# Optimization experiments

Hardware: AMD Instinct MI355X
Metric: run time of the kernel (lower is better)

Reference implementation:

```python
import jax, jax.numpy as jnp
import numpy as np

N = 2_097_152
NUM_DIM = 4
NUM_FACTOR = 32
VOCABS = {"dow": 7, "time": 24, "sex": 2, "age": 100, "month": 12, "day": 31}
NUM_DEST = 100_000


def setup_inputs() -> dict:
    key = jax.random.key(0)
    ks = jax.random.split(key, 16)
    inp = {}
    # forward index args
    names = ["dayofweek", "time", "sex", "age", "month", "day"]
    maxes = [7, 24, 2, 100, 12, 31]
    for i, (n, m) in enumerate(zip(names, maxes)):
        inp[n] = jax.random.randint(ks[i], (N,), 0, m, dtype=jnp.int64 if jax.config.jax_enable_x64 else jnp.int32)
    inp["destination"] = jax.random.randint(ks[6], (N,), 0, NUM_DEST, dtype=jnp.int32)
    # learned params (all feature embeddings ~ N(0,1) like nn.init.normal_)
    inp["emb_dow"] = jax.random.normal(ks[7], (7, NUM_DIM), jnp.float32)
    inp["emb_time"] = jax.random.normal(ks[8], (24, NUM_DIM), jnp.float32)
    inp["emb_sex"] = jax.random.normal(ks[9], (2, NUM_DIM), jnp.float32)
    inp["emb_age"] = jax.random.normal(ks[10], (100, NUM_DIM), jnp.float32)
    inp["emb_month"] = jax.random.normal(ks[11], (12, NUM_DIM), jnp.float32)
    inp["emb_day"] = jax.random.normal(ks[12], (31, NUM_DIM), jnp.float32)
    # user projection Linear(6*num_dim -> num_factor)
    fan_in = 6 * NUM_DIM
    bound = 1.0 / np.sqrt(fan_in)
    inp["W"] = jax.random.uniform(ks[13], (fan_in, NUM_FACTOR), jnp.float32, -bound, bound)
    inp["b"] = jax.random.uniform(ks[14], (NUM_FACTOR,), jnp.float32, -bound, bound)
    inp["item_table"] = jax.random.normal(ks[15], (NUM_DEST, NUM_FACTOR), jnp.float32)
    return inp


def reference(dayofweek, time, sex, age, month, day, destination,
              emb_dow, emb_time, emb_sex, emb_age, emb_month, emb_day,
              W, b, item_table):
    # user embedding: gather 6 feature embeddings, concat -> [N, 24], project -> [N, 32]
    u = jnp.concatenate([
        emb_dow[dayofweek], emb_time[time], emb_sex[sex],
        emb_age[age], emb_month[month], emb_day[day],
    ], axis=-1)
    user = u @ W + b                      # [N, F]
    item = item_table[destination]        # [N, F]
    # diag(user @ item^T) == row-wise dot product (same math, O(N) not O(N^2))
    return jnp.sum(user * item, axis=-1)  # [N]
```

## Files before the change

kernel.cpp:

```cpp
#include <hip/hip_runtime.h>


#define NF 32
#define LDS_STRIDE 36
#define NV 176

__device__ __forceinline__ float4 ldsf4(const float* p) {
    return *reinterpret_cast<const float4*>(p);
}

__device__ __forceinline__ float dot4(float4 u, float4 v, float a) {
    a = fmaf(u.x, v.x, a);
    a = fmaf(u.y, v.y, a);
    a = fmaf(u.z, v.z, a);
    a = fmaf(u.w, v.w, a);
    return a;
}

#define QUAD(IV, Q)                                                  \
    acc0 = dot4(ldsf4(&proj[b0 + (Q) * 4]), IV, acc0);               \
    acc1 = dot4(ldsf4(&proj[b1 + (Q) * 4]), IV, acc1);               \
    acc2 = dot4(ldsf4(&proj[b2 + (Q) * 4]), IV, acc2);               \
    acc0 = dot4(ldsf4(&proj[b3 + (Q) * 4]), IV, acc0);               \
    acc1 = dot4(ldsf4(&proj[b4 + (Q) * 4]), IV, acc1);               \
    acc2 = dot4(ldsf4(&proj[b5 + (Q) * 4]), IV, acc2);

#define NTL(P) __builtin_nontemporal_load(P)

__global__ __launch_bounds__(256, 4)
void mf_kernel(const int* __restrict__ dow, const int* __restrict__ tmi,
               const int* __restrict__ sx,  const int* __restrict__ ag,
               const int* __restrict__ mo,  const int* __restrict__ dy,
               const int* __restrict__ dst,
               const float* __restrict__ e_dow,   const float* __restrict__ e_time,
               const float* __restrict__ e_sex,   const float* __restrict__ e_age,
               const float* __restrict__ e_month, const float* __restrict__ e_day,
               const float* __restrict__ W, const float* __restrict__ bvec,
               const float* __restrict__ item_table,
               float* __restrict__ out, int n)
{
    __shared__ float proj[NV * LDS_STRIDE];

    const int tid = threadIdx.x;
    for (int t = tid; t < NV * NF; t += blockDim.x) {
        int entry = t >> 5;
        int f     = t & 31;
        int k, v;
        const float* e;
        if      (entry < 7)   { k = 0; v = entry;       e = e_dow;   }
        else if (entry < 31)  { k = 1; v = entry - 7;   e = e_time;  }
        else if (entry < 33)  { k = 2; v = entry - 31;  e = e_sex;   }
        else if (entry < 133) { k = 3; v = entry - 33;  e = e_age;   }
        else if (entry < 145) { k = 4; v = entry - 133; e = e_month; }
        else                  { k = 5; v = entry - 145; e = e_day;   }
        float acc = (k == 0) ? bvec[f] : 0.0f;
        #pragma unroll
        for (int d = 0; d < 4; ++d)
            acc += e[v * 4 + d] * W[(k * 4 + d) * NF + f];
        proj[entry * LDS_STRIDE + f] = acc;
    }
    __syncthreads();

    const int tstride = gridDim.x * blockDim.x;
    int i = blockIdx.x * blockDim.x + tid;
    if (i >= n) return;

    int j0 = NTL(&dow[i]), j1 = NTL(&tmi[i]), j2 = NTL(&sx[i]),
        j3 = NTL(&ag[i]),  j4 = NTL(&mo[i]),  j5 = NTL(&dy[i]),
        jd = NTL(&dst[i]);

    for (;;) {
        const int b0 = (0   + j0) * LDS_STRIDE;
        const int b1 = (7   + j1) * LDS_STRIDE;
        const int b2 = (31  + j2) * LDS_STRIDE;
        const int b3 = (33  + j3) * LDS_STRIDE;
        const int b4 = (133 + j4) * LDS_STRIDE;
        const int b5 = (145 + j5) * LDS_STRIDE;
        const float4* it = reinterpret_cast<const float4*>(item_table + (long long)jd * NF);

        float4 iv0 = it[0];
        float4 iv1 = it[1];
        float4 iv2 = it[2];
        float4 iv3 = it[3];
        float4 iv4 = it[4];
        float4 iv5 = it[5];
        float4 iv6 = it[6];
        float4 iv7 = it[7];

        const int ni = i + tstride;
        const bool more = ni < n;
        if (more) {
            j0 = NTL(&dow[ni]); j1 = NTL(&tmi[ni]); j2 = NTL(&sx[ni]);
            j3 = NTL(&ag[ni]);  j4 = NTL(&mo[ni]);  j5 = NTL(&dy[ni]);
            jd = NTL(&dst[ni]);
        }

        asm volatile("" ::: "memory");

        float acc0 = 0.0f, acc1 = 0.0f, acc2 = 0.0f;
        QUAD(iv0, 0)
        QUAD(iv1, 1)
        QUAD(iv2, 2)
        QUAD(iv3, 3)
        QUAD(iv4, 4)
        QUAD(iv5, 5)
        QUAD(iv6, 6)
        QUAD(iv7, 7)
        __builtin_nontemporal_store(acc0 + acc1 + acc2, &out[i]);

        if (!more) break;
        i = ni;
    }
}

extern "C" void kernel_launch(void* const* d_in, const int* in_sizes, int n_in,
                              void* d_out, int out_size, void* d_ws, size_t ws_size,
                              hipStream_t stream) {
    const int* dow = (const int*)d_in[0];
    const int* tmi = (const int*)d_in[1];
    const int* sx  = (const int*)d_in[2];
    const int* ag  = (const int*)d_in[3];
    const int* mo  = (const int*)d_in[4];
    const int* dy  = (const int*)d_in[5];
    const int* dst = (const int*)d_in[6];
    const float* e_dow   = (const float*)d_in[7];
    const float* e_time  = (const float*)d_in[8];
    const float* e_sex   = (const float*)d_in[9];
    const float* e_age   = (const float*)d_in[10];
    const float* e_month = (const float*)d_in[11];
    const float* e_day   = (const float*)d_in[12];
    const float* W       = (const float*)d_in[13];
    const float* bvec    = (const float*)d_in[14];
    const float* item    = (const float*)d_in[15];
    float* out = (float*)d_out;
    const int n = in_sizes[0];

    dim3 grid(2048), block(256);
    mf_kernel<<<grid, block, 0, stream>>>(dow, tmi, sx, ag, mo, dy, dst,
                                          e_dow, e_time, e_sex, e_age, e_month, e_day,
                                          W, bvec, item, out, n);
}
```

Baseline: 171.6 us.

## Precombine feature-pair projections into joint LDS tables to cut per-row lookups

Builds combined projected tables for (dow,time) and (sex,month) pairs, so each row does 4 LDS row lookups instead of 6 and fewer FMAs. The LDS table grows to 323 entries and the per-block precompute grows. Blocks become 512 threads with a grid of 1024 and launch bounds of 6 blocks, trading occupancy settings and a larger setup cost. Summation order changes slightly.

```diff
diff --git a/kernel.cpp b/kernel.cpp
--- a/kernel.cpp
+++ b/kernel.cpp
@@ -3,7 +3,10 @@
 
 #define NF 32
 #define LDS_STRIDE 36
-#define NV 176
+#define NV2 323
+#define T1_OFF 168
+#define T2_OFF 192
+#define T3_OFF 292
 
 __device__ __forceinline__ float4 ldsf4(const float* p) {
     return *reinterpret_cast<const float4*>(p);
@@ -21,13 +24,11 @@
     acc0 = dot4(ldsf4(&proj[b0 + (Q) * 4]), IV, acc0);               \
     acc1 = dot4(ldsf4(&proj[b1 + (Q) * 4]), IV, acc1);               \
     acc2 = dot4(ldsf4(&proj[b2 + (Q) * 4]), IV, acc2);               \
-    acc0 = dot4(ldsf4(&proj[b3 + (Q) * 4]), IV, acc0);               \
-    acc1 = dot4(ldsf4(&proj[b4 + (Q) * 4]), IV, acc1);               \
-    acc2 = dot4(ldsf4(&proj[b5 + (Q) * 4]), IV, acc2);
+    acc3 = dot4(ldsf4(&proj[b3 + (Q) * 4]), IV, acc3);
 
 #define NTL(P) __builtin_nontemporal_load(P)
 
-__global__ __launch_bounds__(256, 4)
+__global__ __launch_bounds__(512, 6)
 void mf_kernel(const int* __restrict__ dow, const int* __restrict__ tmi,
                const int* __restrict__ sx,  const int* __restrict__ ag,
                const int* __restrict__ mo,  const int* __restrict__ dy,
@@ -39,24 +40,45 @@
                const float* __restrict__ item_table,
                float* __restrict__ out, int n)
 {
-    __shared__ float proj[NV * LDS_STRIDE];
+    __shared__ float proj[NV2 * LDS_STRIDE];
 
     const int tid = threadIdx.x;
-    for (int t = tid; t < NV * NF; t += blockDim.x) {
-        int entry = t >> 5;
-        int f     = t & 31;
-        int k, v;
-        const float* e;
-        if      (entry < 7)   { k = 0; v = entry;       e = e_dow;   }
-        else if (entry < 31)  { k = 1; v = entry - 7;   e = e_time;  }
-        else if (entry < 33)  { k = 2; v = entry - 31;  e = e_sex;   }
-        else if (entry < 133) { k = 3; v = entry - 33;  e = e_age;   }
-        else if (entry < 145) { k = 4; v = entry - 133; e = e_month; }
-        else                  { k = 5; v = entry - 145; e = e_day;   }
-        float acc = (k == 0) ? bvec[f] : 0.0f;
-        #pragma unroll
-        for (int d = 0; d < 4; ++d)
-            acc += e[v * 4 + d] * W[(k * 4 + d) * NF + f];
+    for (int t = tid; t < NV2 * NF; t += blockDim.x) {
+        const int entry = t >> 5;
+        const int f     = t & 31;
+        float acc;
+        if (entry < T1_OFF) {
+            const int a = entry / 24;
+            const int b = entry - a * 24;
+            acc = bvec[f];
+            #pragma unroll
+            for (int d = 0; d < 4; ++d) {
+                acc = fmaf(e_dow[a * 4 + d],  W[(0  + d) * NF + f], acc);
+                acc = fmaf(e_time[b * 4 + d], W[(4  + d) * NF + f], acc);
+            }
+        } else if (entry < T2_OFF) {
+            const int e2 = entry - T1_OFF;
+            const int a = e2 / 12;
+            const int b = e2 - a * 12;
+            acc = 0.0f;
+            #pragma unroll
+            for (int d = 0; d < 4; ++d) {
+                acc = fmaf(e_sex[a * 4 + d],   W[(8  + d) * NF + f], acc);
+                acc = fmaf(e_month[b * 4 + d], W[(16 + d) * NF + f], acc);
+            }
+        } else if (entry < T3_OFF) {
+            const int v = entry - T2_OFF;
+            acc = 0.0f;
+            #pragma unroll
+            for (int d = 0; d < 4; ++d)
+                acc = fmaf(e_age[v * 4 + d], W[(12 + d) * NF + f], acc);
+        } else {
+            const int v = entry - T3_OFF;
+            acc = 0.0f;
+            #pragma unroll
+            for (int d = 0; d < 4; ++d)
+                acc = fmaf(e_day[v * 4 + d], W[(20 + d) * NF + f], acc);
+        }
         proj[entry * LDS_STRIDE + f] = acc;
     }
     __syncthreads();
@@ -70,12 +92,10 @@
         jd = NTL(&dst[i]);
 
     for (;;) {
-        const int b0 = (0   + j0) * LDS_STRIDE;
-        const int b1 = (7   + j1) * LDS_STRIDE;
-        const int b2 = (31  + j2) * LDS_STRIDE;
-        const int b3 = (33  + j3) * LDS_STRIDE;
-        const int b4 = (133 + j4) * LDS_STRIDE;
-        const int b5 = (145 + j5) * LDS_STRIDE;
+        const int b0 = (j0 * 24 + j1) * LDS_STRIDE;
+        const int b1 = (T1_OFF + j2 * 12 + j4) * LDS_STRIDE;
+        const int b2 = (T2_OFF + j3) * LDS_STRIDE;
+        const int b3 = (T3_OFF + j5) * LDS_STRIDE;
         const float4* it = reinterpret_cast<const float4*>(item_table + (long long)jd * NF);
 
         float4 iv0 = it[0];
@@ -97,7 +117,7 @@
 
         asm volatile("" ::: "memory");
 
-        float acc0 = 0.0f, acc1 = 0.0f, acc2 = 0.0f;
+        float acc0 = 0.0f, acc1 = 0.0f, acc2 = 0.0f, acc3 = 0.0f;
         QUAD(iv0, 0)
         QUAD(iv1, 1)
         QUAD(iv2, 2)
@@ -106,7 +126,7 @@
         QUAD(iv5, 5)
         QUAD(iv6, 6)
         QUAD(iv7, 7)
-        __builtin_nontemporal_store(acc0 + acc1 + acc2, &out[i]);
+        __builtin_nontemporal_store((acc0 + acc1) + (acc2 + acc3), &out[i]);
 
         if (!more) break;
         i = ni;
@@ -135,7 +155,7 @@
     float* out = (float*)d_out;
     const int n = in_sizes[0];
 
-    dim3 grid(2048), block(256);
+    dim3 grid(1024), block(512);
     mf_kernel<<<grid, block, 0, stream>>>(dow, tmi, sx, ag, mo, dy, dst,
                                           e_dow, e_time, e_sex, e_age, e_month, e_day,
                                           W, bvec, item, out, n);
```

After: 187.8 us. 1.09x slower.
